# Kernel tuning notes

Hardware: AMD Instinct MI355X
Metric: run time of the kernel (lower is better)

## Reference

```python
import jax, jax.numpy as jnp
import numpy as np

B, N, D, H, DK, MS, FF = 8, 256, 256, 16, 16, 16, 512
EPS = 1e-5


def _inorm(x, scale, bias):
    # InstanceNorm1d over the node dim (axis=1) per channel, affine
    m = jnp.mean(x, axis=1, keepdims=True)
    v = jnp.var(x, axis=1, keepdims=True)
    return (x - m) * jax.lax.rsqrt(v + EPS) * scale + bias


def _heads(x):
    b, n, _ = x.shape
    return x.reshape(b, n, H, DK).transpose(0, 2, 1, 3)  # (b,H,n,DK)


def _block(emb_r, emb_c, cost, Wq, Wk, Wv, m1w, m1b, m2w, m2b, cw, cb,
           n1s, n1b, w1, b1, w2, b2, n2s, n2b):
    b, n, _ = emb_r.shape
    q = _heads(emb_r @ Wq)
    k = _heads(emb_c @ Wk)
    v = _heads(emb_c @ Wv)
    dot = jnp.einsum('bhid,bhjd->bhij', q, k) / jnp.sqrt(jnp.float32(DK))
    # stack dot-product score with cost-matrix score: (b,H,r,c,2)
    two = jnp.stack([dot, jnp.broadcast_to(cost[:, None], dot.shape)], axis=-1)
    # per-head 2 -> MS -> 1 MLP on each (row,col) score pair
    ms1 = jax.nn.relu(jnp.einsum('bhrcs,hsm->bhrcm', two, m1w)
                      + m1b[None, :, None, None, :])
    mixed = jnp.einsum('bhrcm,hm->bhrc', ms1, m2w[:, :, 0]) \
            + m2b[:, 0][None, :, None, None]
    w = jax.nn.softmax(mixed, axis=-1)
    out = jnp.einsum('bhrc,bhcd->bhrd', w, v)
    out_concat = out.transpose(0, 2, 1, 3).reshape(b, n, H * DK)
    mh = out_concat @ cw + cb
    out1 = _inorm(emb_r + mh, n1s, n1b)
    ff = jax.nn.relu(out1 @ w1 + b1) @ w2 + b2
    return _inorm(out1 + ff, n2s, n2b)


def setup_inputs() -> dict:
    key = jax.random.key(0)
    keys = iter(jax.random.split(key, 64))
    def nrm(shape, s=0.05):
        return jax.random.normal(next(keys), shape, dtype=jnp.float32) * s
    inp = {
        'row_emb': nrm((B, N, D), 1.0),
        'col_emb': nrm((B, N, D), 1.0),
        'cost_mat': jax.random.uniform(next(keys), (B, N, N), dtype=jnp.float32),
    }
    for p in ('r', 'c'):
        inp[p + 'Wq'] = nrm((D, H * DK)); inp[p + 'Wk'] = nrm((D, H * DK)); inp[p + 'Wv'] = nrm((D, H * DK))
        inp[p + 'm1w'] = nrm((H, 2, MS), 0.5); inp[p + 'm1b'] = nrm((H, MS), 0.5)
        inp[p + 'm2w'] = nrm((H, MS, 1), 0.25); inp[p + 'm2b'] = nrm((H, 1), 0.25)
        inp[p + 'cw'] = nrm((H * DK, D)); inp[p + 'cb'] = jnp.zeros((D,), jnp.float32)
        inp[p + 'n1s'] = jnp.ones((D,), jnp.float32); inp[p + 'n1b'] = jnp.zeros((D,), jnp.float32)
        inp[p + 'w1'] = nrm((D, FF)); inp[p + 'b1'] = jnp.zeros((FF,), jnp.float32)
        inp[p + 'w2'] = nrm((FF, D)); inp[p + 'b2'] = jnp.zeros((D,), jnp.float32)
        inp[p + 'n2s'] = jnp.ones((D,), jnp.float32); inp[p + 'n2b'] = jnp.zeros((D,), jnp.float32)
    return inp


def reference(row_emb, col_emb, cost_mat,
              rWq, rWk, rWv, rm1w, rm1b, rm2w, rm2b, rcw, rcb,
              rn1s, rn1b, rw1, rb1, rw2, rb2, rn2s, rn2b,
              cWq, cWk, cWv, cm1w, cm1b, cm2w, cm2b, ccw, ccb,
              cn1s, cn1b, cw1, cb1, cw2, cb2, cn2s, cn2b):
    row_out = _block(row_emb, col_emb, cost_mat,
                     rWq, rWk, rWv, rm1w, rm1b, rm2w, rm2b, rcw, rcb,
                     rn1s, rn1b, rw1, rb1, rw2, rb2, rn2s, rn2b)
    col_out = _block(col_emb, row_emb, cost_mat.transpose(0, 2, 1),
                     cWq, cWk, cWv, cm1w, cm1b, cm2w, cm2b, ccw, ccb,
                     cn1s, cn1b, cw1, cb1, cw2, cb2, cn2s, cn2b)
    return row_out, col_out
```

## Files before the change

### kernel.cpp

```cpp
#include <hip/hip_runtime.h>
#include <hip/hip_bf16.h>

#define Bc 8
#define Nc 256
#define Dc 256
#define Hc 16
#define DKc 16
#define MSc 16
#define FFc 512
#define SZc 524288
#define WHALF 524288
#define FFH 1048576

typedef __hip_bfloat16 bf16;
typedef __attribute__((ext_vector_type(8))) short bfrag8;
typedef __attribute__((ext_vector_type(4))) float f32x4;

__device__ __forceinline__ short f2bs(float x) {
    bf16 t = __float2bfloat16(x);
    return *reinterpret_cast<short*>(&t);
}

__global__ void setup_kernel(const float* __restrict__ e0, const float* __restrict__ e1,
                             bf16* __restrict__ o0, bf16* __restrict__ o1,
                             float* __restrict__ statsB,
                             const float* rWq, const float* rWk, const float* rWv,
                             const float* rcw, const float* rw1, const float* rw2,
                             const float* cWq, const float* cWk, const float* cWv,
                             const float* ccw, const float* cw1, const float* cw2,
                             bf16* __restrict__ WT) {
    int y = blockIdx.y;
    if (y < 2) {
        const float* src = y ? e1 : e0;
        bf16* dst = y ? o1 : o0;
        size_t base = (size_t)blockIdx.x * 2048 + threadIdx.x;
#pragma unroll
        for (int i = 0; i < 8; ++i)
            dst[base + i * 256] = __float2bfloat16(src[base + i * 256]);
        return;
    }
    if (y == 2) {
        if (blockIdx.x < 64) statsB[blockIdx.x * 256 + threadIdx.x] = 0.f;
        return;
    }
    int z = y - 3;
    int p = z / 6, widx = z % 6;
    const float* src; int K, N; size_t off;
    switch (widx) {
        case 0: src = p ? cWq : rWq; K = 256; N = 256; off = 0; break;
        case 1: src = p ? cWk : rWk; K = 256; N = 256; off = 65536; break;
        case 2: src = p ? cWv : rWv; K = 256; N = 256; off = 131072; break;
        case 3: src = p ? ccw : rcw; K = 256; N = 256; off = 196608; break;
        case 4: src = p ? cw1 : rw1; K = 256; N = 512; off = 262144; break;
        default: src = p ? cw2 : rw2; K = 512; N = 256; off = 393216; break;
    }
    int Ntiles = N >> 5, Ktiles = K >> 5;
    if ((int)blockIdx.x >= Ktiles * Ntiles) return;
    int kt = blockIdx.x / Ntiles, nt = blockIdx.x - kt * Ntiles;
    int k0 = kt * 32, n0 = nt * 32;
    bf16* dst = WT + (size_t)p * WHALF + off;
    __shared__ float t[32][33];
    int tx = threadIdx.x & 31, ty = threadIdx.x >> 5;
#pragma unroll
    for (int i = 0; i < 4; ++i)
        t[ty + i * 8][tx] = src[(size_t)(k0 + ty + i * 8) * N + n0 + tx];
    __syncthreads();
#pragma unroll
    for (int i = 0; i < 4; ++i)
        dst[(size_t)(n0 + ty + i * 8) * K + k0 + tx] = __float2bfloat16(t[tx][ty + i * 8]);
}

__device__ __forceinline__ void mfma_loop(const short* pa0, const short* pa1,
                                          const short* pb, int K,
                                          f32x4& acc0, f32x4& acc1) {
    for (int kt = 0; kt < K; kt += 32) {
        bfrag8 a0 = *(const bfrag8*)(pa0 + kt);
        bfrag8 a1 = *(const bfrag8*)(pa1 + kt);
        bfrag8 b  = *(const bfrag8*)(pb + kt);
        acc0 = __builtin_amdgcn_mfma_f32_16x16x32_bf16(a0, b, acc0, 0, 0, 0);
        acc1 = __builtin_amdgcn_mfma_f32_16x16x32_bf16(a1, b, acc1, 0, 0, 0);
    }
}

__global__ void gemm_qkv_kernel(const short* __restrict__ embRb, const short* __restrict__ embCb,
                                const short* __restrict__ WT, float* __restrict__ qkv) {
    int z = blockIdx.z;
    int p = z / 3, j = z % 3;
    const short* A  = (j == 0) ? (p ? embCb : embRb) : (p ? embRb : embCb);
    const short* BT = WT + (size_t)p * WHALF + j * 65536;
    float* out = qkv + (size_t)z * SZc;

    int lane = threadIdx.x & 63, w = threadIdx.x >> 6;
    int m_base = blockIdx.x * 64 + (w & 1) * 32;
    int n_base = blockIdx.y * 32 + (w >> 1) * 16;
    int mr = lane & 15, quad = lane >> 4;

    const short* pa0 = A + (size_t)(m_base + mr) * 256 + quad * 8;
    const short* pa1 = pa0 + 16 * 256;
    const short* pb  = BT + (size_t)(n_base + mr) * 256 + quad * 8;

    f32x4 acc0 = {0.f, 0.f, 0.f, 0.f}, acc1 = {0.f, 0.f, 0.f, 0.f};
    mfma_loop(pa0, pa1, pb, 256, acc0, acc1);

    int col = n_base + mr;
    int h = col >> 4, dk = col & 15;
#pragma unroll
    for (int r = 0; r < 4; ++r) {
        int row0 = m_base + quad * 4 + r;
        int row1 = row0 + 16;
        int b0 = row0 >> 8, n0 = row0 & 255;
        int b1 = row1 >> 8, n1 = row1 & 255;
        out[((size_t)(b0 * Hc + h) * Nc + n0) * DKc + dk] = acc0[r];
        out[((size_t)(b1 * Hc + h) * Nc + n1) * DKc + dk] = acc1[r];
    }
}

__global__ void attn_kernel(const float* __restrict__ qkv, const float* __restrict__ cost,
                            const float* rm1w, const float* rm1b,
                            const float* rm2w, const float* rm2b,
                            const float* cm1w, const float* cm1b,
                            const float* cm2w, const float* cm2b,
                            bf16* __restrict__ attnb) {
    int b = blockIdx.x, h = blockIdx.y;
    int p = blockIdx.z >> 4, rc = blockIdx.z & 15;
    int tr = p;
    const float* Q = qkv + (size_t)(p * 3 + 0) * SZc;
    const float* K = qkv + (size_t)(p * 3 + 1) * SZc;
    const float* V = qkv + (size_t)(p * 3 + 2) * SZc;
    const float* m1w = p ? cm1w : rm1w;
    const float* m1b = p ? cm1b : rm1b;
    const float* m2w = p ? cm2w : rm2w;
    const float* m2b = p ? cm2b : rm2b;
    bf16* out_concat = attnb + (size_t)p * SZc;

    int bh = b * Hc + h;
    int r0 = rc * 16;
    int c = threadIdx.x;
    int lane = c & 63, wid = c >> 6;

    __shared__ __align__(16) short sVT[16 * 264];
    __shared__ __align__(16) short sEb[16 * 264];
    __shared__ float sQ[16][16];
    __shared__ float sPart[4 * 256];
    __shared__ float sSum[16 * 4];
    __shared__ float sm1w[32], sm1b[16], sm2w[16], sm2bS[1];

    float kreg[16];
    {
        const float* kp = K + ((size_t)bh * Nc + c) * DKc;
        const float* vp = V + ((size_t)bh * Nc + c) * DKc;
#pragma unroll
        for (int i = 0; i < 4; ++i) {
            float4 kv = *(const float4*)(kp + i * 4);
            float4 vv = *(const float4*)(vp + i * 4);
            kreg[i * 4]     = kv.x; kreg[i * 4 + 1] = kv.y;
            kreg[i * 4 + 2] = kv.z; kreg[i * 4 + 3] = kv.w;
            sVT[(i * 4 + 0) * 264 + c] = f2bs(vv.x);
            sVT[(i * 4 + 1) * 264 + c] = f2bs(vv.y);
            sVT[(i * 4 + 2) * 264 + c] = f2bs(vv.z);
            sVT[(i * 4 + 3) * 264 + c] = f2bs(vv.w);
        }
    }
    if (c < 64) {
        float4 qv = *(const float4*)(Q + ((size_t)bh * Nc + r0) * DKc + c * 4);
        int rl = c >> 2, off = (c & 3) * 4;
        sQ[rl][off] = qv.x; sQ[rl][off + 1] = qv.y;
        sQ[rl][off + 2] = qv.z; sQ[rl][off + 3] = qv.w;
    } else if (c < 96)   sm1w[c - 64]  = m1w[h * 32 + (c - 64)];
    else if (c < 112)    sm1b[c - 96]  = m1b[h * 16 + (c - 96)];
    else if (c < 128)    sm2w[c - 112] = m2w[h * 16 + (c - 112)];
    else if (c == 128)   sm2bS[0] = m2b[h];
    __syncthreads();

    const float* costR = cost + (size_t)b * Nc * Nc;
    float creg[16];
    if (tr) {
#pragma unroll
        for (int g = 0; g < 4; ++g) {
            float4 cv = *(const float4*)(costR + (size_t)c * Nc + r0 + g * 4);
            creg[g * 4]     = cv.x; creg[g * 4 + 1] = cv.y;
            creg[g * 4 + 2] = cv.z; creg[g * 4 + 3] = cv.w;
        }
    }

    for (int rl = 0; rl < 16; ++rl) {
        float dot = 0.f;
#pragma unroll
        for (int k = 0; k < 16; ++k) dot += kreg[k] * sQ[rl][k];
        dot *= 0.25f;
        float cost_v = tr ? creg[rl] : costR[(size_t)(r0 + rl) * Nc + c];
        float mixed = sm2bS[0];
#pragma unroll
        for (int m = 0; m < MSc; ++m) {
            float t = fmaf(dot, sm1w[m], fmaf(cost_v, sm1w[16 + m], sm1b[m]));
            t = fmaxf(t, 0.f);
            mixed = fmaf(t, sm2w[m], mixed);
        }
        float e = __expf(mixed);
        sEb[rl * 264 + c] = f2bs(e);
        float s = e;
#pragma unroll
        for (int off = 32; off > 0; off >>= 1) s += __shfl_xor(s, off);
        if (lane == 0) sSum[rl * 4 + wid] = s;
    }
    __syncthreads();

    {
        int mr = lane & 15, quad = lane >> 4;
        const short* pa = &sEb[mr * 264 + wid * 64 + quad * 8];
        const short* pb = &sVT[mr * 264 + wid * 64 + quad * 8];
        f32x4 acc = {0.f, 0.f, 0.f, 0.f};
        bfrag8 a0 = *(const bfrag8*)pa;
        bfrag8 b0 = *(const bfrag8*)pb;
        acc = __builtin_amdgcn_mfma_f32_16x16x32_bf16(a0, b0, acc, 0, 0, 0);
        bfrag8 a1 = *(const bfrag8*)(pa + 32);
        bfrag8 b1 = *(const bfrag8*)(pb + 32);
        acc = __builtin_amdgcn_mfma_f32_16x16x32_bf16(a1, b1, acc, 0, 0, 0);
#pragma unroll
        for (int r = 0; r < 4; ++r)
            sPart[wid * 256 + (quad * 4 + r) * 16 + mr] = acc[r];
    }
    __syncthreads();

    {
        int r = c >> 4, dk = c & 15;
        float o = sPart[c] + sPart[256 + c] + sPart[512 + c] + sPart[768 + c];
        float sum = sSum[r * 4] + sSum[r * 4 + 1] + sSum[r * 4 + 2] + sSum[r * 4 + 3];
        out_concat[((size_t)(b * Nc + r0 + r)) * Dc + h * DKc + dk] =
            __float2bfloat16(o / sum);
    }
}

__global__ void gemm_cat_kernel(const short* __restrict__ attnb, const short* __restrict__ WT,
                                const float* rcb, const float* ccb,
                                const float* __restrict__ resR, const float* __restrict__ resC,
                                float* __restrict__ x1, float* __restrict__ stats1) {
    int p = blockIdx.z;
    const short* A  = attnb + (size_t)p * SZc;
    const short* BT = WT + (size_t)p * WHALF + 196608;
    const float* bias = p ? ccb : rcb;
    const float* res  = p ? resC : resR;
    float* outF = x1 + (size_t)p * SZc;
    float* st   = stats1 + p * 4096;

    int lane = threadIdx.x & 63, w = threadIdx.x >> 6;
    int m_base = blockIdx.x * 64 + (w & 1) * 32;
    int n_base = blockIdx.y * 32 + (w >> 1) * 16;
    int mr = lane & 15, quad = lane >> 4;

    const short* pa0 = A + (size_t)(m_base + mr) * 256 + quad * 8;
    const short* pa1 = pa0 + (size_t)16 * 256;
    const short* pb  = BT + (size_t)(n_base + mr) * 256 + quad * 8;

    f32x4 acc0 = {0.f, 0.f, 0.f, 0.f}, acc1 = {0.f, 0.f, 0.f, 0.f};
    mfma_loop(pa0, pa1, pb, 256, acc0, acc1);

    int col = n_base + mr;
    float bv = bias[col];
    int bb = m_base >> 8;
    float ssum = 0.f, ssq = 0.f;
#pragma unroll
    for (int r = 0; r < 4; ++r) {
        int row0 = m_base + quad * 4 + r;
        int row1 = row0 + 16;
        float v0 = acc0[r] + bv + res[(size_t)row0 * 256 + col];
        float v1 = acc1[r] + bv + res[(size_t)row1 * 256 + col];
        outF[(size_t)row0 * 256 + col] = v0;
        outF[(size_t)row1 * 256 + col] = v1;
        ssum += v0 + v1;
        ssq  += v0 * v0 + v1 * v1;
    }
    atomicAdd(&st[(bb * 256 + col) * 2],     ssum);
    atomicAdd(&st[(bb * 256 + col) * 2 + 1], ssq);
}

__global__ __launch_bounds__(256) void gemm_ff1n_kernel(
        const float* __restrict__ x1, const float* __restrict__ stats1,
        const float* rn1s, const float* rn1b, const float* cn1s, const float* cn1b,
        const short* __restrict__ WT, const float* rb1, const float* cb1,
        bf16* __restrict__ ffh) {
    int p = blockIdx.z;
    const float* X   = x1 + (size_t)p * SZc;
    const float* st  = stats1 + p * 4096;
    const float* n1s = p ? cn1s : rn1s;
    const float* n1b = p ? cn1b : rn1b;
    const short* BT  = WT + (size_t)p * WHALF + 262144;
    const float* bias = p ? cb1 : rb1;
    bf16* outB = ffh + (size_t)p * FFH;

    __shared__ __align__(16) short sA[64 * 264];
    int c = threadIdx.x;
    int m_base = blockIdx.x * 64;
    int b = m_base >> 8;

    float s = st[(b * 256 + c) * 2];
    float q = st[(b * 256 + c) * 2 + 1];
    float mean = s * (1.f / Nc);
    float var = q * (1.f / Nc) - mean * mean;
    float inv = rsqrtf(var + 1e-5f) * n1s[c];
    float nb = n1b[c];
#pragma unroll 8
    for (int i = 0; i < 64; ++i) {
        float v = X[(size_t)(m_base + i) * 256 + c];
        sA[i * 264 + c] = f2bs((v - mean) * inv + nb);
    }
    __syncthreads();

    int lane = c & 63, w = c >> 6;
    int mloc = (w & 1) * 32;
    int n_base = blockIdx.y * 32 + (w >> 1) * 16;
    int mr = lane & 15, quad = lane >> 4;

    const short* pa0 = &sA[(mloc + mr) * 264 + quad * 8];
    const short* pa1 = pa0 + 16 * 264;
    const short* pb  = BT + (size_t)(n_base + mr) * 256 + quad * 8;

    f32x4 acc0 = {0.f, 0.f, 0.f, 0.f}, acc1 = {0.f, 0.f, 0.f, 0.f};
#pragma unroll
    for (int kt = 0; kt < 256; kt += 32) {
        bfrag8 a0 = *(const bfrag8*)(pa0 + kt);
        bfrag8 a1 = *(const bfrag8*)(pa1 + kt);
        bfrag8 bb = *(const bfrag8*)(pb + kt);
        acc0 = __builtin_amdgcn_mfma_f32_16x16x32_bf16(a0, bb, acc0, 0, 0, 0);
        acc1 = __builtin_amdgcn_mfma_f32_16x16x32_bf16(a1, bb, acc1, 0, 0, 0);
    }

    int col = n_base + mr;
    float bv = bias[col];
#pragma unroll
    for (int r = 0; r < 4; ++r) {
        int row0 = m_base + mloc + quad * 4 + r;
        int row1 = row0 + 16;
        outB[(size_t)row0 * 512 + col] = __float2bfloat16(fmaxf(acc0[r] + bv, 0.f));
        outB[(size_t)row1 * 512 + col] = __float2bfloat16(fmaxf(acc1[r] + bv, 0.f));
    }
}

__global__ void gemm_ff2n_kernel(const short* __restrict__ ffh, const short* __restrict__ WT,
                                 const float* rb2, const float* cb2,
                                 const float* __restrict__ x1, const float* __restrict__ stats1,
                                 const float* rn1s, const float* rn1b,
                                 const float* cn1s, const float* cn1b,
                                 float* __restrict__ ff2, float* __restrict__ stats2) {
    int p = blockIdx.z;
    const short* A  = ffh + (size_t)p * FFH;
    const short* BT = WT + (size_t)p * WHALF + 393216;
    const float* bias = p ? cb2 : rb2;
    const float* X   = x1 + (size_t)p * SZc;
    const float* st1 = stats1 + p * 4096;
    const float* n1s = p ? cn1s : rn1s;
    const float* n1b = p ? cn1b : rn1b;
    float* outF = ff2 + (size_t)p * SZc;
    float* st2  = stats2 + p * 4096;

    int lane = threadIdx.x & 63, w = threadIdx.x >> 6;
    int m_base = blockIdx.x * 64 + (w & 1) * 32;
    int n_base = blockIdx.y * 32 + (w >> 1) * 16;
    int mr = lane & 15, quad = lane >> 4;

    const short* pa0 = A + (size_t)(m_base + mr) * 512 + quad * 8;
    const short* pa1 = pa0 + (size_t)16 * 512;
    const short* pb  = BT + (size_t)(n_base + mr) * 512 + quad * 8;

    f32x4 acc0 = {0.f, 0.f, 0.f, 0.f}, acc1 = {0.f, 0.f, 0.f, 0.f};
    mfma_loop(pa0, pa1, pb, 512, acc0, acc1);

    int col = n_base + mr;
    int bb = m_base >> 8;
    float s1 = st1[(bb * 256 + col) * 2];
    float q1 = st1[(bb * 256 + col) * 2 + 1];
    float mean1 = s1 * (1.f / Nc);
    float var1 = q1 * (1.f / Nc) - mean1 * mean1;
    float inv1 = rsqrtf(var1 + 1e-5f) * n1s[col];
    float nb1 = n1b[col];
    float bv = bias[col];

    float ssum = 0.f, ssq = 0.f;
#pragma unroll
    for (int r = 0; r < 4; ++r) {
        int row0 = m_base + quad * 4 + r;
        int row1 = row0 + 16;
        float res0 = (X[(size_t)row0 * 256 + col] - mean1) * inv1 + nb1;
        float res1 = (X[(size_t)row1 * 256 + col] - mean1) * inv1 + nb1;
        float v0 = acc0[r] + bv + res0;
        float v1 = acc1[r] + bv + res1;
        outF[(size_t)row0 * 256 + col] = v0;
        outF[(size_t)row1 * 256 + col] = v1;
        ssum += v0 + v1;
        ssq  += v0 * v0 + v1 * v1;
    }
    atomicAdd(&st2[(bb * 256 + col) * 2],     ssum);
    atomicAdd(&st2[(bb * 256 + col) * 2 + 1], ssq);
}

__global__ void apply_kernel(const float* __restrict__ x, const float* __restrict__ stats,
                             const float* sR, const float* bR,
                             const float* sC, const float* bC,
                             float* __restrict__ outF) {
    int p = blockIdx.y;
    int row = blockIdx.x;
    int b = row >> 8;
    int d = threadIdx.x;
    const float* st = stats + p * 4096;
    float sum = st[(b * 256 + d) * 2];
    float sq  = st[(b * 256 + d) * 2 + 1];
    float mean = sum * (1.f / Nc);
    float var = sq * (1.f / Nc) - mean * mean;
    float inv = rsqrtf(var + 1e-5f);
    float scale = (p ? sC : sR)[d];
    float bias  = (p ? bC : bR)[d];
    float v = x[(size_t)p * SZc + (size_t)row * Dc + d];
    outF[(size_t)p * SZc + (size_t)row * Dc + d] = (v - mean) * inv * scale + bias;
}

extern "C" void kernel_launch(void* const* d_in, const int* in_sizes, int n_in,
                              void* d_out, int out_size, void* d_ws, size_t ws_size,
                              hipStream_t stream) {
    const float* row_emb = (const float*)d_in[0];
    const float* col_emb = (const float*)d_in[1];
    const float* cost    = (const float*)d_in[2];
    float* out = (float*)d_out;
    float* ws = (float*)d_ws;
#define RP(i) ((const float*)d_in[3 + (i)])
#define CP(i) ((const float*)d_in[20 + (i)])

    float* qkv    = ws;
    float* x1     = ws + 6 * (size_t)SZc;
    float* ff2    = ws + 8 * (size_t)SZc;
    float* statsB = ws + 10 * (size_t)SZc;
    bf16* bfbase  = (bf16*)(statsB + 16384);
    bf16* embRb = bfbase;
    bf16* embCb = embRb + SZc;
    bf16* attnb = embCb + SZc;
    bf16* ffh   = attnb + 2 * (size_t)SZc;
    bf16* WT    = ffh + 4 * (size_t)SZc;
    float* stats1 = statsB;
    float* stats2 = statsB + 8192;

    setup_kernel<<<dim3(256, 15), 256, 0, stream>>>(
        row_emb, col_emb, embRb, embCb, statsB,
        RP(0), RP(1), RP(2), RP(7), RP(11), RP(13),
        CP(0), CP(1), CP(2), CP(7), CP(11), CP(13), WT);
    gemm_qkv_kernel<<<dim3(32, 8, 6), 256, 0, stream>>>(
        (const short*)embRb, (const short*)embCb, (const short*)WT, qkv);
    attn_kernel<<<dim3(Bc, Hc, 32), 256, 0, stream>>>(
        qkv, cost, RP(3), RP(4), RP(5), RP(6), CP(3), CP(4), CP(5), CP(6), attnb);
    gemm_cat_kernel<<<dim3(32, 8, 2), 256, 0, stream>>>(
        (const short*)attnb, (const short*)WT, RP(8), CP(8), row_emb, col_emb, x1, stats1);
    gemm_ff1n_kernel<<<dim3(32, 16, 2), 256, 0, stream>>>(
        x1, stats1, RP(9), RP(10), CP(9), CP(10),
        (const short*)WT, RP(12), CP(12), ffh);
    gemm_ff2n_kernel<<<dim3(32, 8, 2), 256, 0, stream>>>(
        (const short*)ffh, (const short*)WT, RP(14), CP(14),
        x1, stats1, RP(9), RP(10), CP(9), CP(10), ff2, stats2);
    apply_kernel<<<dim3(2048, 2), 256, 0, stream>>>(
        ff2, stats2, RP(15), RP(16), CP(15), CP(16), out);
#undef RP
#undef CP
}
```

Baseline: 243.1 us.

## Compute attention QK scores with bf16 MFMA and restructure score-MLP per MFMA tile

Replaces the per-thread scalar Q·K dot products (16 rows per column thread) with bf16 16x16x32 MFMA instructions, padding the K dimension to 32 with zeros. The score MLP, exp and row-sum reduction are reorganized to operate on the MFMA output layout, with row sums done via 16-lane shuffles instead of full-wave reductions. Cost-matrix loads are remapped to that layout. This cuts scalar FMA and shuffle work but rounds Q and K to bf16, which lowers score precision and may change the cost-matrix access coalescing.

```diff
diff --git a/kernel.cpp b/kernel.cpp
--- a/kernel.cpp
+++ b/kernel.cpp
@@ -123,7 +123,6 @@
                             bf16* __restrict__ attnb) {
     int b = blockIdx.x, h = blockIdx.y;
     int p = blockIdx.z >> 4, rc = blockIdx.z & 15;
-    int tr = p;
     const float* Q = qkv + (size_t)(p * 3 + 0) * SZc;
     const float* K = qkv + (size_t)(p * 3 + 1) * SZc;
     const float* V = qkv + (size_t)(p * 3 + 2) * SZc;
@@ -137,76 +136,115 @@
     int r0 = rc * 16;
     int c = threadIdx.x;
     int lane = c & 63, wid = c >> 6;
+    int mr = lane & 15, quad = lane >> 4;
 
     __shared__ __align__(16) short sVT[16 * 264];
     __shared__ __align__(16) short sEb[16 * 264];
-    __shared__ float sQ[16][16];
     __shared__ float sPart[4 * 256];
     __shared__ float sSum[16 * 4];
     __shared__ float sm1w[32], sm1b[16], sm2w[16], sm2bS[1];
 
-    float kreg[16];
     {
-        const float* kp = K + ((size_t)bh * Nc + c) * DKc;
         const float* vp = V + ((size_t)bh * Nc + c) * DKc;
 #pragma unroll
         for (int i = 0; i < 4; ++i) {
-            float4 kv = *(const float4*)(kp + i * 4);
             float4 vv = *(const float4*)(vp + i * 4);
-            kreg[i * 4]     = kv.x; kreg[i * 4 + 1] = kv.y;
-            kreg[i * 4 + 2] = kv.z; kreg[i * 4 + 3] = kv.w;
             sVT[(i * 4 + 0) * 264 + c] = f2bs(vv.x);
             sVT[(i * 4 + 1) * 264 + c] = f2bs(vv.y);
             sVT[(i * 4 + 2) * 264 + c] = f2bs(vv.z);
             sVT[(i * 4 + 3) * 264 + c] = f2bs(vv.w);
         }
     }
-    if (c < 64) {
-        float4 qv = *(const float4*)(Q + ((size_t)bh * Nc + r0) * DKc + c * 4);
-        int rl = c >> 2, off = (c & 3) * 4;
-        sQ[rl][off] = qv.x; sQ[rl][off + 1] = qv.y;
-        sQ[rl][off + 2] = qv.z; sQ[rl][off + 3] = qv.w;
-    } else if (c < 96)   sm1w[c - 64]  = m1w[h * 32 + (c - 64)];
-    else if (c < 112)    sm1b[c - 96]  = m1b[h * 16 + (c - 96)];
-    else if (c < 128)    sm2w[c - 112] = m2w[h * 16 + (c - 112)];
-    else if (c == 128)   sm2bS[0] = m2b[h];
+    if (c >= 64 && c < 96)  sm1w[c - 64]  = m1w[h * 32 + (c - 64)];
+    else if (c >= 96 && c < 112)  sm1b[c - 96]  = m1b[h * 16 + (c - 96)];
+    else if (c >= 112 && c < 128) sm2w[c - 112] = m2w[h * 16 + (c - 112)];
+    else if (c == 128)            sm2bS[0] = m2b[h];
+
+    bfrag8 qf = {0, 0, 0, 0, 0, 0, 0, 0};
+    if (quad < 2) {
+        const float* qp = Q + ((size_t)bh * Nc + r0 + mr) * DKc + quad * 8;
+        float4 qa = *(const float4*)qp;
+        float4 qb = *(const float4*)(qp + 4);
+        qf[0] = f2bs(qa.x); qf[1] = f2bs(qa.y); qf[2] = f2bs(qa.z); qf[3] = f2bs(qa.w);
+        qf[4] = f2bs(qb.x); qf[5] = f2bs(qb.y); qf[6] = f2bs(qb.z); qf[7] = f2bs(qb.w);
+    }
+
+    float sv[16];
+#pragma unroll
+    for (int t = 0; t < 4; ++t) {
+        bfrag8 kf = {0, 0, 0, 0, 0, 0, 0, 0};
+        if (quad < 2) {
+            const float* kp = K + ((size_t)bh * Nc + wid * 64 + t * 16 + mr) * DKc + quad * 8;
+            float4 ka = *(const float4*)kp;
+            float4 kb = *(const float4*)(kp + 4);
+            kf[0] = f2bs(ka.x); kf[1] = f2bs(ka.y); kf[2] = f2bs(ka.z); kf[3] = f2bs(ka.w);
+            kf[4] = f2bs(kb.x); kf[5] = f2bs(kb.y); kf[6] = f2bs(kb.z); kf[7] = f2bs(kb.w);
+        }
+        f32x4 acc = {0.f, 0.f, 0.f, 0.f};
+        acc = __builtin_amdgcn_mfma_f32_16x16x32_bf16(qf, kf, acc, 0, 0, 0);
+        sv[t * 4 + 0] = acc[0] * 0.25f;
+        sv[t * 4 + 1] = acc[1] * 0.25f;
+        sv[t * 4 + 2] = acc[2] * 0.25f;
+        sv[t * 4 + 3] = acc[3] * 0.25f;
+    }
+
+    const float* costR = cost + (size_t)b * Nc * Nc;
+    float cv[16];
+    if (p) {
+#pragma unroll
+        for (int t = 0; t < 4; ++t) {
+            float4 cvv = *(const float4*)(costR +
+                (size_t)(wid * 64 + t * 16 + mr) * Nc + r0 + quad * 4);
+            cv[t * 4 + 0] = cvv.x; cv[t * 4 + 1] = cvv.y;
+            cv[t * 4 + 2] = cvv.z; cv[t * 4 + 3] = cvv.w;
+        }
+    } else {
+#pragma unroll
+        for (int t = 0; t < 4; ++t)
+#pragma unroll
+            for (int r = 0; r < 4; ++r)
+                cv[t * 4 + r] = costR[(size_t)(r0 + quad * 4 + r) * Nc +
+                                      wid * 64 + t * 16 + mr];
+    }
+
     __syncthreads();
 
-    const float* costR = cost + (size_t)b * Nc * Nc;
-    float creg[16];
-    if (tr) {
-#pragma unroll
-        for (int g = 0; g < 4; ++g) {
-            float4 cv = *(const float4*)(costR + (size_t)c * Nc + r0 + g * 4);
-            creg[g * 4]     = cv.x; creg[g * 4 + 1] = cv.y;
-            creg[g * 4 + 2] = cv.z; creg[g * 4 + 3] = cv.w;
+    float mix[16] = {0.f, 0.f, 0.f, 0.f, 0.f, 0.f, 0.f, 0.f,
+                     0.f, 0.f, 0.f, 0.f, 0.f, 0.f, 0.f, 0.f};
+    for (int m = 0; m < MSc; ++m) {
+        float w1d = sm1w[m];
+        float w1c = sm1w[16 + m];
+        float b1v = sm1b[m];
+        float w2v = sm2w[m];
+#pragma unroll
+        for (int s = 0; s < 16; ++s) {
+            float tt = fmaf(sv[s], w1d, fmaf(cv[s], w1c, b1v));
+            mix[s] = fmaf(fmaxf(tt, 0.f), w2v, mix[s]);
         }
     }
-
-    for (int rl = 0; rl < 16; ++rl) {
-        float dot = 0.f;
-#pragma unroll
-        for (int k = 0; k < 16; ++k) dot += kreg[k] * sQ[rl][k];
-        dot *= 0.25f;
-        float cost_v = tr ? creg[rl] : costR[(size_t)(r0 + rl) * Nc + c];
-        float mixed = sm2bS[0];
-#pragma unroll
-        for (int m = 0; m < MSc; ++m) {
-            float t = fmaf(dot, sm1w[m], fmaf(cost_v, sm1w[16 + m], sm1b[m]));
-            t = fmaxf(t, 0.f);
-            mixed = fmaf(t, sm2w[m], mixed);
-        }
-        float e = __expf(mixed);
-        sEb[rl * 264 + c] = f2bs(e);
-        float s = e;
-#pragma unroll
-        for (int off = 32; off > 0; off >>= 1) s += __shfl_xor(s, off);
-        if (lane == 0) sSum[rl * 4 + wid] = s;
+    float b2v = sm2bS[0];
+    float ex[16];
+#pragma unroll
+    for (int s = 0; s < 16; ++s) ex[s] = __expf(mix[s] + b2v);
+
+#pragma unroll
+    for (int t = 0; t < 4; ++t)
+#pragma unroll
+        for (int r = 0; r < 4; ++r)
+            sEb[(quad * 4 + r) * 264 + wid * 64 + t * 16 + mr] = f2bs(ex[t * 4 + r]);
+
+#pragma unroll
+    for (int r = 0; r < 4; ++r) {
+        float rp = ex[r] + ex[4 + r] + ex[8 + r] + ex[12 + r];
+        rp += __shfl_xor(rp, 1);
+        rp += __shfl_xor(rp, 2);
+        rp += __shfl_xor(rp, 4);
+        rp += __shfl_xor(rp, 8);
+        if (mr == 0) sSum[(quad * 4 + r) * 4 + wid] = rp;
     }
     __syncthreads();
 
     {
-        int mr = lane & 15, quad = lane >> 4;
         const short* pa = &sEb[mr * 264 + wid * 64 + quad * 8];
         const short* pb = &sVT[mr * 264 + wid * 64 + quad * 8];
         f32x4 acc = {0.f, 0.f, 0.f, 0.f};
```

After: 231.2 us. 4.9% less time.
